# Performance work log

Hardware: AMD Instinct MI355X
Metric: run time of the kernel (lower is better)

## Reference

```python
import jax, jax.numpy as jnp
import numpy as np

B, S, D, H = 4, 2048, 1024, 16
DK = D // H  # 64
THETA = 10000.0


def _rope(x, pos):
    # x: [..., s, d], pos: [s] int. Rotation-matrix RoPE applied to consecutive pairs.
    d = x.shape[-1]
    inv_freq = 1.0 / (THETA ** (jnp.arange(0, d, 2, dtype=jnp.float32) / d))  # [d/2]
    freqs = pos.astype(jnp.float32)[:, None] * inv_freq[None, :]             # [s, d/2]
    cos, sin = jnp.cos(freqs), jnp.sin(freqs)
    xr = x.reshape(x.shape[:-1] + (d // 2, 2))
    x0, x1 = xr[..., 0], xr[..., 1]
    y0 = cos * x0 - sin * x1
    y1 = sin * x0 + cos * x1
    return jnp.stack([y0, y1], axis=-1).reshape(x.shape)


def setup_inputs() -> dict:
    key = jax.random.key(0)
    ks = jax.random.split(key, 5)
    std = float(np.sqrt(2.0 / (D + D)))
    return {
        "x": jax.random.normal(ks[0], (B, S, D), dtype=jnp.float32),
        "token_positions": jnp.arange(S, dtype=jnp.int32),
        "wq": jax.random.normal(ks[1], (D, D), dtype=jnp.float32) * std,
        "wk": jax.random.normal(ks[2], (D, D), dtype=jnp.float32) * std,
        "wv": jax.random.normal(ks[3], (D, D), dtype=jnp.float32) * std,
        "wo": jax.random.normal(ks[4], (D, D), dtype=jnp.float32) * std,
    }


def reference(x, token_positions, wq, wk, wv, wo):
    # Linear layers use weight [out, in]: y = x @ W^T
    q = jnp.einsum('bsd,od->bso', x, wq).reshape(B, S, H, DK).transpose(0, 2, 1, 3)  # [b,h,s,dk]
    k = jnp.einsum('bsd,od->bso', x, wk).reshape(B, S, H, DK).transpose(0, 2, 1, 3)
    v = jnp.einsum('bsd,od->bso', x, wv).reshape(B, S, H, DK).transpose(0, 2, 1, 3)
    q = _rope(q, token_positions)
    k = _rope(k, token_positions)
    scores = jnp.einsum('bhqd,bhkd->bhqk', q, k) / jnp.sqrt(jnp.float32(DK))
    causal = jnp.tril(jnp.ones((S, S), dtype=bool))
    scores = jnp.where(causal, scores, jnp.finfo(scores.dtype).min)
    attn = jax.nn.softmax(scores, axis=-1)
    o = jnp.einsum('bhqk,bhkd->bhqd', attn, v)          # [b,h,s,dk]
    o = o.transpose(0, 2, 1, 3).reshape(B, S, D)        # [b,s,h*dk]
    return jnp.einsum('bsd,od->bso', o, wo)
```

## Files before the change

### kernel.cpp

```cpp
#include <hip/hip_runtime.h>
#include <hip/hip_bf16.h>
#include <stdint.h>

#define S_LEN 2048
#define NHEAD 16
#define BATCH 4

typedef __attribute__((ext_vector_type(8))) short short8;
typedef __attribute__((ext_vector_type(4))) float f32x4;
typedef __attribute__((ext_vector_type(4))) unsigned short u16x4;

__device__ float2 g_tab[131072];

__device__ __forceinline__ unsigned short f2bf(float f) {
  union { float f; uint32_t u; } a; a.f = f;
  uint32_t r = (a.u + 0x7fff + ((a.u >> 16) & 1)) >> 16;
  return (unsigned short)r;
}
__device__ __forceinline__ float bf2f(unsigned short u) {
  union { uint32_t u; float f; } a; a.u = ((uint32_t)u) << 16;
  return a.f;
}
__device__ __forceinline__ uint32_t pk2bf(float a, float b) {
  union { __hip_bfloat162 h; uint32_t u; } cv;
  cv.h = __float22bfloat162_rn(float2{a, b});
  return cv.u;
}

__device__ __forceinline__ void gload16(const void* g, void* l) {
  __builtin_amdgcn_global_load_lds(
      (const __attribute__((address_space(1))) void*)g,
      (__attribute__((address_space(3))) void*)l, 16, 0, 0);
}

__device__ __forceinline__ short8 rope8(short8 v, float4 t01, float4 t23) {
  float x0 = bf2f((unsigned short)v[0]), x1 = bf2f((unsigned short)v[1]);
  float x2 = bf2f((unsigned short)v[2]), x3 = bf2f((unsigned short)v[3]);
  float x4 = bf2f((unsigned short)v[4]), x5 = bf2f((unsigned short)v[5]);
  float x6 = bf2f((unsigned short)v[6]), x7 = bf2f((unsigned short)v[7]);
  union { uint32_t u[4]; short8 v; } o;
  o.u[0] = pk2bf(t01.x * x0 - t01.y * x1, t01.y * x0 + t01.x * x1);
  o.u[1] = pk2bf(t01.z * x2 - t01.w * x3, t01.w * x2 + t01.z * x3);
  o.u[2] = pk2bf(t23.x * x4 - t23.y * x5, t23.y * x4 + t23.x * x5);
  o.u[3] = pk2bf(t23.z * x6 - t23.w * x7, t23.w * x6 + t23.z * x7);
  return o.v;
}

__global__ void k_prep(const float* __restrict__ x, const float* __restrict__ wq,
                       const float* __restrict__ wk, const float* __restrict__ wv,
                       const float* __restrict__ wo, const int* __restrict__ pos,
                       unsigned short* __restrict__ xb, unsigned short* __restrict__ wdst) {
  int bid = blockIdx.x;
  if (bid < 8192) {
    int i = bid * 256 + threadIdx.x;
    float4 v = ((const float4*)x)[i];
    union { uint32_t u[2]; u16x4 v; } o;
    o.u[0] = pk2bf(v.x, v.y);
    o.u[1] = pk2bf(v.z, v.w);
    ((u16x4*)xb)[i] = o.v;
  } else if (bid < 12288) {
    int i = (bid - 8192) * 256 + threadIdx.x;
    int r = i >> 18;
    const float* s = r == 0 ? wq : r == 1 ? wk : r == 2 ? wv : wo;
    float4 v = ((const float4*)s)[i & 0x3FFFF];
    union { uint32_t u[2]; u16x4 v; } o;
    o.u[0] = pk2bf(v.x, v.y);
    o.u[1] = pk2bf(v.z, v.w);
    ((u16x4*)wdst)[i] = o.v;
  } else {
    int i = (bid - 12288) * 256 + threadIdx.x;
    int s = i >> 5, p = i & 31;
    float fp = (float)pos[s];
    float inv = exp2f(-(float)p * 0.41524101186092029f);
    float sn, cs;
    __sincosf(fp * inv, &sn, &cs);
    const float SCL = 0.18033688011112042f;
    g_tab[i] = float2{cs * SCL, sn * SCL};
    g_tab[65536 + i] = float2{cs, sn};
  }
}

template<int OUTF32>
__global__ __launch_bounds__(256) void k_gemm_nt(
    const unsigned short* __restrict__ A, const unsigned short* __restrict__ B,
    void* __restrict__ Cp, int K, int ldc, int gx)
{
  __shared__ unsigned short lA[2][128 * 64];
  __shared__ unsigned short lB[2][128 * 64];
  const int tid = threadIdx.x;
  const int w = tid >> 6, lane = tid & 63;
  const int wm = w >> 1, wn = w & 1;
  const int l15 = lane & 15, lg = lane >> 4;
  const int nwg = (int)gridDim.x, slot = (int)blockIdx.x;
  const int f = (slot & 7) * (nwg >> 3) + (slot >> 3);
  const int row0 = (f / gx) * 128, col0 = (f % gx) * 128;

  f32x4 acc[4][4] = {};
  const size_t rsb = (size_t)K * 2;

  auto stage = [&](int buf, int k0) {
#pragma unroll
    for (int it = 0; it < 4; ++it) {
      int fb = w * 4096 + it * 1024 + lane * 16;
      int r = fb >> 7, cb = fb & 127;
      gload16((const char*)A + (size_t)(row0 + r) * rsb + k0 * 2 + cb,
              (char*)(&lA[buf][0]) + (w * 4096 + it * 1024));
      gload16((const char*)B + (size_t)(col0 + r) * rsb + k0 * 2 + cb,
              (char*)(&lB[buf][0]) + (w * 4096 + it * 1024));
    }
  };

  const int nk = K >> 6;
  stage(0, 0);
  __syncthreads();

  for (int t = 0; t < nk; ++t) {
    const int cur = t & 1;
    if (t + 1 < nk) stage(cur ^ 1, (t + 1) * 64);

#pragma unroll
    for (int ks = 0; ks < 2; ++ks) {
      short8 af[4], bg[4];
#pragma unroll
      for (int i = 0; i < 4; ++i) {
        int rowa = wm * 64 + i * 16 + l15;
        af[i] = *(const short8*)((const char*)(&lA[cur][0]) + rowa * 128 + ks * 64 + lg * 16);
        int rowb = wn * 64 + i * 16 + l15;
        bg[i] = *(const short8*)((const char*)(&lB[cur][0]) + rowb * 128 + ks * 64 + lg * 16);
      }
#pragma unroll
      for (int i = 0; i < 4; ++i)
#pragma unroll
        for (int j = 0; j < 4; ++j)
          acc[i][j] = __builtin_amdgcn_mfma_f32_16x16x32_bf16(af[i], bg[j], acc[i][j], 0, 0, 0);
    }
    __syncthreads();
  }

#pragma unroll
  for (int i = 0; i < 4; ++i)
#pragma unroll
    for (int j = 0; j < 4; ++j) {
      int col = col0 + wn * 64 + j * 16 + l15;
#pragma unroll
      for (int r = 0; r < 4; ++r) {
        int row = row0 + wm * 64 + i * 16 + lg * 4 + r;
        float v = acc[i][j][r];
        if (OUTF32) ((float*)Cp)[(size_t)row * ldc + col] = v;
        else ((unsigned short*)Cp)[(size_t)row * ldc + col] = f2bf(v);
      }
    }
}

__global__ void k_rope(unsigned short* __restrict__ qkv) {
  int idx = blockIdx.x * 256 + threadIdx.x;
  int row = idx >> 7;
  int cq = idx & 127;
  int s = row & (S_LEN - 1);
  const float4* tb = (const float4*)&g_tab[65536 + s * 32 + ((cq * 4) & 31)];
  float4 t0 = tb[0], t1 = tb[1];
  size_t off = (size_t)row * 3072 + 1024 + cq * 8;
  short8 v = *(short8*)(qkv + off);
  *(short8*)(qkv + off) = rope8(v, t0, t1);
}

__global__ __launch_bounds__(512) void k_attn(const unsigned short* __restrict__ qkv,
                                              unsigned short* __restrict__ O) {
  __shared__ unsigned short lK[2][64 * 64];
  __shared__ uint32_t lV32[2][64 * 36];

  const int tid = threadIdx.x, w = tid >> 6, lane = tid & 63;
  const int l15 = lane & 15, lg = lane >> 4;
  const int slot = (int)blockIdx.x;
  const int f0 = (slot & 7) * 128 + (slot >> 3);
  const int bh = f0 >> 4, qt = f0 & 15;
  const int b = bh >> 4, h = bh & 15;
  const size_t rstride = 3072;

  const int D = (w < 4) ? (31 - qt) : qt;
  const int wa = w & 3;
  const int qrow = D * 64 + wa * 16 + l15;
  const int NT = 32 - qt;

  short8 vr;

  auto stageK = [&](int buf, int t) {
    int fb = tid * 16;
    int r = fb >> 7;
    int cb = (fb ^ ((r & 7) << 4)) & 127;
    gload16((const char*)qkv + ((size_t)(b * S_LEN + t * 64 + r) * rstride + 1024 + h * 64) * 2 + cb,
            (char*)(&lK[buf][0]) + fb);
  };
  auto loadV = [&](int t) {
    int kp = tid >> 4, sub = tid & 15;
    int pp = sub & 1, c = (sub >> 1) * 8;
    vr = *(const short8*)(qkv + (size_t)(b * S_LEN + t * 64 + kp * 2 + pp) * rstride + 2048 + h * 64 + c);
  };
  auto writeV = [&](int buf) {
    int kp = tid >> 4, sub = tid & 15;
    int pp = sub & 1, c = (sub >> 1) * 8;
    uint32_t u0 = __shfl_xor(((const uint32_t*)&vr)[0], 1);
    uint32_t u1 = __shfl_xor(((const uint32_t*)&vr)[1], 1);
    uint32_t u2 = __shfl_xor(((const uint32_t*)&vr)[2], 1);
    uint32_t u3 = __shfl_xor(((const uint32_t*)&vr)[3], 1);
    unsigned short ov[8];
    ((uint32_t*)ov)[0] = u0; ((uint32_t*)ov)[1] = u1;
    ((uint32_t*)ov)[2] = u2; ((uint32_t*)ov)[3] = u3;
    const unsigned short* own = (const unsigned short*)&vr;
    int colk = ((kp >> 4) << 4) | (((kp >> 1) & 3) << 2) | (((kp >> 3) & 1) << 1) | (kp & 1);
#pragma unroll
    for (int j = 0; j < 4; ++j) {
      int d = c + (pp ? 4 : 0) + j;
      unsigned short lo = pp ? ov[4 + j] : own[j];
      unsigned short hi = pp ? own[4 + j] : ov[j];
      uint32_t packed = (uint32_t)lo | ((uint32_t)hi << 16);
      int colS = colk ^ (((d >> 3) & 7) << 2);
      lV32[buf][d * 36 + colS] = packed;
    }
  };

  short8 ones;
#pragma unroll
  for (int e = 0; e < 8; ++e) ones[e] = (short)0x3F80;

  short8 qf[2];
  {
    const unsigned short* qpt = qkv + (size_t)(b * S_LEN + qrow) * rstride + h * 64 + lg * 8;
    short8 q0 = *(const short8*)qpt;
    short8 q1 = *(const short8*)(qpt + 32);
    const float4* t0p = (const float4*)&g_tab[qrow * 32 + lg * 4];
    const float4* t1p = (const float4*)&g_tab[qrow * 32 + 16 + lg * 4];
    qf[0] = rope8(q0, t0p[0], t0p[1]);
    qf[1] = rope8(q1, t1p[0], t1p[1]);
  }

  float mrun = 0.f;
  f32x4 oacc[4] = {};
  f32x4 csum = {};

  stageK(0, 0);
  loadV(0);
  writeV(0);
  __syncthreads();

  for (int t = 0; t < NT; ++t) {
    const int cur = t & 1, nxt = cur ^ 1;
    const bool more = (t + 1 < NT);
    if (more) { stageK(nxt, t + 1); loadV(t + 1); }

    const bool active = (t <= D);
    if (active) {
      f32x4 sf[4] = {};
      __builtin_amdgcn_s_setprio(1);
#pragma unroll
      for (int ks = 0; ks < 2; ++ks) {
#pragma unroll
        for (int jf = 0; jf < 4; ++jf) {
          int krow = jf * 16 + l15;
          int g = krow * 128 + ks * 64 + lg * 16;
          int a = g ^ ((krow & 7) << 4);
          short8 kb = *(const short8*)((const char*)(&lK[cur][0]) + a);
          sf[jf] = __builtin_amdgcn_mfma_f32_16x16x32_bf16(kb, qf[ks], sf[jf], 0, 0, 0);
        }
      }
      __builtin_amdgcn_s_setprio(0);

      const bool dg = (t == D);
      float pv[4][4];
#pragma unroll
      for (int jf = 0; jf < 4; ++jf)
#pragma unroll
        for (int r = 0; r < 4; ++r) {
          float v = sf[jf][r];
          if (dg) {
            int kglob = t * 64 + jf * 16 + lg * 4 + r;
            if (kglob > qrow) v = -3e38f;
          }
          pv[jf][r] = v;
        }
      if (t == 0) {
        float mx = -3e38f;
#pragma unroll
        for (int jf = 0; jf < 4; ++jf)
#pragma unroll
          for (int r = 0; r < 4; ++r) mx = fmaxf(mx, pv[jf][r]);
        mx = fmaxf(mx, __shfl_xor(mx, 16));
        mx = fmaxf(mx, __shfl_xor(mx, 32));
        mrun = mx;
      }
#pragma unroll
      for (int jf = 0; jf < 4; ++jf)
#pragma unroll
        for (int r = 0; r < 4; ++r)
          pv[jf][r] = exp2f(pv[jf][r] - mrun);

      __builtin_amdgcn_s_setprio(1);
#pragma unroll
      for (int ks = 0; ks < 2; ++ks) {
        union { uint32_t u[4]; short8 v; } pb;
        pb.u[0] = pk2bf(pv[2 * ks][0], pv[2 * ks][1]);
        pb.u[1] = pk2bf(pv[2 * ks][2], pv[2 * ks][3]);
        pb.u[2] = pk2bf(pv[2 * ks + 1][0], pv[2 * ks + 1][1]);
        pb.u[3] = pk2bf(pv[2 * ks + 1][2], pv[2 * ks + 1][3]);
#pragma unroll
        for (int j = 0; j < 4; ++j) {
          int d = j * 16 + l15;
          int colS = (ks * 16 + lg * 4) ^ (((d >> 3) & 7) << 2);
          short8 vb = *(const short8*)(&lV32[cur][d * 36 + colS]);
          oacc[j] = __builtin_amdgcn_mfma_f32_16x16x32_bf16(vb, pb.v, oacc[j], 0, 0, 0);
        }
        csum = __builtin_amdgcn_mfma_f32_16x16x32_bf16(ones, pb.v, csum, 0, 0, 0);
      }
      __builtin_amdgcn_s_setprio(0);
    }

    if (more) writeV(nxt);
    __syncthreads();

    if (active) {
      if (!__all(csum[0] <= 1.0e9f)) {
        const float al = 0x1p-32f;
#pragma unroll
        for (int j = 0; j < 4; ++j)
#pragma unroll
          for (int r = 0; r < 4; ++r) oacc[j][r] *= al;
#pragma unroll
        for (int r = 0; r < 4; ++r) csum[r] *= al;
        mrun += 32.0f;
      }
    }
  }

  float rinv = __builtin_amdgcn_rcpf(csum[0]);
  unsigned short* orow = O + (size_t)(b * S_LEN + qrow) * 1024 + h * 64;
#pragma unroll
  for (int j = 0; j < 4; ++j) {
    union { uint32_t u[2]; u16x4 v; } ow;
    ow.u[0] = pk2bf(oacc[j][0] * rinv, oacc[j][1] * rinv);
    ow.u[1] = pk2bf(oacc[j][2] * rinv, oacc[j][3] * rinv);
    *(u16x4*)(orow + j * 16 + lg * 4) = ow.v;
  }
}

extern "C" void kernel_launch(void* const* d_in, const int* in_sizes, int n_in,
                              void* d_out, int out_size, void* d_ws, size_t ws_size,
                              hipStream_t stream) {
  const float* x  = (const float*)d_in[0];
  const int* pos  = (const int*)d_in[1];
  const float* wq = (const float*)d_in[2];
  const float* wk = (const float*)d_in[3];
  const float* wv = (const float*)d_in[4];
  const float* wo = (const float*)d_in[5];
  float* out = (float*)d_out;

  char* ws = (char*)d_ws;
  unsigned short* xb   = (unsigned short*)(ws);
  unsigned short* wqkv = (unsigned short*)(ws + (size_t)16 * 1024 * 1024);
  unsigned short* wob  = (unsigned short*)(ws + (size_t)22 * 1024 * 1024);
  unsigned short* qkv  = (unsigned short*)(ws + (size_t)24 * 1024 * 1024);
  unsigned short* ob   = (unsigned short*)(ws + (size_t)72 * 1024 * 1024);

  k_prep<<<12544, 256, 0, stream>>>(x, wq, wk, wv, wo, pos, xb, wqkv);

  k_gemm_nt<0><<<1536, 256, 0, stream>>>(xb, wqkv, qkv, 1024, 3072, 24);

  k_rope<<<4096, 256, 0, stream>>>(qkv);

  k_attn<<<1024, 512, 0, stream>>>(qkv, ob);

  k_gemm_nt<1><<<512, 256, 0, stream>>>(ob, wob, out, 1024, 1024, 8);
}
```

Measured before the change: 297.6 us.

## Process paired 128-row causal query blocks per workgroup to share K/V tiles

Each attention workgroup now owns two 128-row query blocks, one from the top and one from the bottom of the causal triangle. All 8 waves compute both blocks against each staged K/V tile, so every LDS K fragment feeds two MFMAs and the grid is halved. The aim is to cut global and LDS traffic per FLOP and keep work balanced across blocks. The cost is doubled accumulator registers per thread, hinted by launch_bounds(512,4), and a rewritten diagonal-mask condition that may be looser than before and could affect correctness.

```diff
diff --git a/kernel.cpp b/kernel.cpp
--- a/kernel.cpp
+++ b/kernel.cpp
@@ -164,23 +164,22 @@
   *(short8*)(qkv + off) = rope8(v, t0, t1);
 }
 
-__global__ __launch_bounds__(512) void k_attn(const unsigned short* __restrict__ qkv,
-                                              unsigned short* __restrict__ O) {
+__global__ __launch_bounds__(512, 4) void k_attn(const unsigned short* __restrict__ qkv,
+                                                 unsigned short* __restrict__ O) {
   __shared__ unsigned short lK[2][64 * 64];
   __shared__ uint32_t lV32[2][64 * 36];
 
   const int tid = threadIdx.x, w = tid >> 6, lane = tid & 63;
   const int l15 = lane & 15, lg = lane >> 4;
   const int slot = (int)blockIdx.x;
-  const int f0 = (slot & 7) * 128 + (slot >> 3);
-  const int bh = f0 >> 4, qt = f0 & 15;
+  const int f0 = (slot & 7) * 64 + (slot >> 3);
+  const int bh = f0 >> 3, qp = f0 & 7;
   const int b = bh >> 4, h = bh & 15;
   const size_t rstride = 3072;
 
-  const int D = (w < 4) ? (31 - qt) : qt;
-  const int wa = w & 3;
-  const int qrow = D * 64 + wa * 16 + l15;
-  const int NT = 32 - qt;
+  const int qbH = (15 - qp) * 128, qbL = qp * 128;
+  const int NT = (qbH >> 6) + 2;
+  const int DL = (qbL >> 6) + 1;
 
   short8 vr;
 
@@ -223,20 +222,26 @@
 #pragma unroll
   for (int e = 0; e < 8; ++e) ones[e] = (short)0x3F80;
 
-  short8 qf[2];
+  const int qrowH = qbH + w * 16 + l15;
+  const int qrowL = qbL + w * 16 + l15;
+
+  short8 qfH[2], qfL[2];
   {
-    const unsigned short* qpt = qkv + (size_t)(b * S_LEN + qrow) * rstride + h * 64 + lg * 8;
-    short8 q0 = *(const short8*)qpt;
-    short8 q1 = *(const short8*)(qpt + 32);
-    const float4* t0p = (const float4*)&g_tab[qrow * 32 + lg * 4];
-    const float4* t1p = (const float4*)&g_tab[qrow * 32 + 16 + lg * 4];
-    qf[0] = rope8(q0, t0p[0], t0p[1]);
-    qf[1] = rope8(q1, t1p[0], t1p[1]);
-  }
-
-  float mrun = 0.f;
-  f32x4 oacc[4] = {};
-  f32x4 csum = {};
+    const unsigned short* qh = qkv + (size_t)(b * S_LEN + qrowH) * rstride + h * 64 + lg * 8;
+    const unsigned short* ql = qkv + (size_t)(b * S_LEN + qrowL) * rstride + h * 64 + lg * 8;
+    const float4* th0 = (const float4*)&g_tab[qrowH * 32 + lg * 4];
+    const float4* th1 = (const float4*)&g_tab[qrowH * 32 + 16 + lg * 4];
+    const float4* tl0 = (const float4*)&g_tab[qrowL * 32 + lg * 4];
+    const float4* tl1 = (const float4*)&g_tab[qrowL * 32 + 16 + lg * 4];
+    qfH[0] = rope8(*(const short8*)qh, th0[0], th0[1]);
+    qfH[1] = rope8(*(const short8*)(qh + 32), th1[0], th1[1]);
+    qfL[0] = rope8(*(const short8*)ql, tl0[0], tl0[1]);
+    qfL[1] = rope8(*(const short8*)(ql + 32), tl1[0], tl1[1]);
+  }
+
+  float mrunH = 0.f, mrunL = 0.f;
+  f32x4 oaccH[4] = {}, oaccL[4] = {};
+  f32x4 csumH = {}, csumL = {};
 
   stageK(0, 0);
   loadV(0);
@@ -248,24 +253,38 @@
     const bool more = (t + 1 < NT);
     if (more) { stageK(nxt, t + 1); loadV(t + 1); }
 
-    const bool active = (t <= D);
-    if (active) {
-      f32x4 sf[4] = {};
-      __builtin_amdgcn_s_setprio(1);
-#pragma unroll
-      for (int ks = 0; ks < 2; ++ks) {
+    const bool actL = (t <= DL);
+
+    f32x4 sfH[4] = {}, sfL[4] = {};
+    __builtin_amdgcn_s_setprio(1);
+    if (actL) {
+#pragma unroll
+      for (int ks = 0; ks < 2; ++ks)
 #pragma unroll
         for (int jf = 0; jf < 4; ++jf) {
           int krow = jf * 16 + l15;
           int g = krow * 128 + ks * 64 + lg * 16;
           int a = g ^ ((krow & 7) << 4);
           short8 kb = *(const short8*)((const char*)(&lK[cur][0]) + a);
-          sf[jf] = __builtin_amdgcn_mfma_f32_16x16x32_bf16(kb, qf[ks], sf[jf], 0, 0, 0);
+          sfH[jf] = __builtin_amdgcn_mfma_f32_16x16x32_bf16(kb, qfH[ks], sfH[jf], 0, 0, 0);
+          sfL[jf] = __builtin_amdgcn_mfma_f32_16x16x32_bf16(kb, qfL[ks], sfL[jf], 0, 0, 0);
         }
-      }
-      __builtin_amdgcn_s_setprio(0);
-
-      const bool dg = (t == D);
+    } else {
+#pragma unroll
+      for (int ks = 0; ks < 2; ++ks)
+#pragma unroll
+        for (int jf = 0; jf < 4; ++jf) {
+          int krow = jf * 16 + l15;
+          int g = krow * 128 + ks * 64 + lg * 16;
+          int a = g ^ ((krow & 7) << 4);
+          short8 kb = *(const short8*)((const char*)(&lK[cur][0]) + a);
+          sfH[jf] = __builtin_amdgcn_mfma_f32_16x16x32_bf16(kb, qfH[ks], sfH[jf], 0, 0, 0);
+        }
+    }
+    __builtin_amdgcn_s_setprio(0);
+
+    auto sm_pv = [&](f32x4 (&sf)[4], float& mrun, f32x4 (&oacc)[4], f32x4& csum, int qrow) {
+      const bool dg = (t * 64 + 63 > qrow - l15 + (w & 0) * 0 + 0 * 64) && (t * 64 + 63 > ((qrow / 16) * 16));
       float pv[4][4];
 #pragma unroll
       for (int jf = 0; jf < 4; ++jf)
@@ -312,33 +331,57 @@
         csum = __builtin_amdgcn_mfma_f32_16x16x32_bf16(ones, pb.v, csum, 0, 0, 0);
       }
       __builtin_amdgcn_s_setprio(0);
-    }
+    };
+
+    sm_pv(sfH, mrunH, oaccH, csumH, qrowH);
+    if (actL) sm_pv(sfL, mrunL, oaccL, csumL, qrowL);
 
     if (more) writeV(nxt);
     __syncthreads();
 
-    if (active) {
-      if (!__all(csum[0] <= 1.0e9f)) {
-        const float al = 0x1p-32f;
-#pragma unroll
-        for (int j = 0; j < 4; ++j)
-#pragma unroll
-          for (int r = 0; r < 4; ++r) oacc[j][r] *= al;
-#pragma unroll
-        for (int r = 0; r < 4; ++r) csum[r] *= al;
-        mrun += 32.0f;
-      }
-    }
-  }
-
-  float rinv = __builtin_amdgcn_rcpf(csum[0]);
-  unsigned short* orow = O + (size_t)(b * S_LEN + qrow) * 1024 + h * 64;
-#pragma unroll
-  for (int j = 0; j < 4; ++j) {
-    union { uint32_t u[2]; u16x4 v; } ow;
-    ow.u[0] = pk2bf(oacc[j][0] * rinv, oacc[j][1] * rinv);
-    ow.u[1] = pk2bf(oacc[j][2] * rinv, oacc[j][3] * rinv);
-    *(u16x4*)(orow + j * 16 + lg * 4) = ow.v;
+    if (!__all(csumH[0] <= 1.0e9f)) {
+      const float al = 0x1p-32f;
+#pragma unroll
+      for (int j = 0; j < 4; ++j)
+#pragma unroll
+        for (int r = 0; r < 4; ++r) oaccH[j][r] *= al;
+#pragma unroll
+      for (int r = 0; r < 4; ++r) csumH[r] *= al;
+      mrunH += 32.0f;
+    }
+    if (!__all(csumL[0] <= 1.0e9f)) {
+      const float al = 0x1p-32f;
+#pragma unroll
+      for (int j = 0; j < 4; ++j)
+#pragma unroll
+        for (int r = 0; r < 4; ++r) oaccL[j][r] *= al;
+#pragma unroll
+      for (int r = 0; r < 4; ++r) csumL[r] *= al;
+      mrunL += 32.0f;
+    }
+  }
+
+  {
+    float rinv = __builtin_amdgcn_rcpf(csumH[0]);
+    unsigned short* orow = O + (size_t)(b * S_LEN + qrowH) * 1024 + h * 64;
+#pragma unroll
+    for (int j = 0; j < 4; ++j) {
+      union { uint32_t u[2]; u16x4 v; } ow;
+      ow.u[0] = pk2bf(oaccH[j][0] * rinv, oaccH[j][1] * rinv);
+      ow.u[1] = pk2bf(oaccH[j][2] * rinv, oaccH[j][3] * rinv);
+      *(u16x4*)(orow + j * 16 + lg * 4) = ow.v;
+    }
+  }
+  {
+    float rinv = __builtin_amdgcn_rcpf(csumL[0]);
+    unsigned short* orow = O + (size_t)(b * S_LEN + qrowL) * 1024 + h * 64;
+#pragma unroll
+    for (int j = 0; j < 4; ++j) {
+      union { uint32_t u[2]; u16x4 v; } ow;
+      ow.u[0] = pk2bf(oaccL[j][0] * rinv, oaccL[j][1] * rinv);
+      ow.u[1] = pk2bf(oaccL[j][2] * rinv, oaccL[j][3] * rinv);
+      *(u16x4*)(orow + j * 16 + lg * 4) = ow.v;
+    }
   }
 }
 
@@ -366,7 +409,7 @@
 
   k_rope<<<4096, 256, 0, stream>>>(qkv);
 
-  k_attn<<<1024, 512, 0, stream>>>(qkv, ob);
+  k_attn<<<512, 512, 0, stream>>>(qkv, ob);
 
   k_gemm_nt<1><<<512, 256, 0, stream>>>(ob, wob, out, 1024, 1024, 8);
 }
```

Result: slower. 476.2 us (+60.0%).
